# Kernel optimization log

Hardware: AMD Instinct MI355X
Metric: run time of the kernel (lower is better)

## Reference

```python
import jax, jax.numpy as jnp
import numpy as np

K_WAVE = 15.0  # wavenumber k from source
EPS_R = 1e-8   # epsilon in dr/dn denominator from source


def bessel_j1(x):
    # Numerical-Recipes rational/asymptotic approximation of J1(x).
    ax = jnp.abs(x)
    y = x * x
    num = x * (72362614232.0 + y * (-7895059235.0 + y * (242396853.1 + y * (-2972611.439 + y * (15704.48260 + y * (-30.16036606))))))
    den = 144725228442.0 + y * (2300535178.0 + y * (18583304.74 + y * (99447.43394 + y * (376.9991397 + y))))
    small = num / den
    axs = jnp.maximum(ax, 1e-20)
    z = 8.0 / axs
    y2 = z * z
    xx = axs - 2.356194491
    p1 = 1.0 + y2 * (0.183105e-2 + y2 * (-0.3516396496e-4 + y2 * (0.2457520174e-5 + y2 * (-0.240337019e-6))))
    p2 = 0.04687499995 + y2 * (-0.2002690873e-3 + y2 * (0.8449199096e-5 + y2 * (-0.88228987e-6 + y2 * 0.105787412e-6)))
    large = jnp.sqrt(0.636619772 / axs) * (jnp.cos(xx) * p1 - z * jnp.sin(xx) * p2) * jnp.sign(x)
    return jnp.where(ax < 8.0, small, large)


def bessel_y1(x):
    # Numerical-Recipes approximation of Y1(x), x > 0.
    xs = jnp.maximum(x, 1e-12)
    y = xs * xs
    num = xs * (-4.900604943e13 + y * (1.275274390e13 + y * (-5.153438139e11 + y * (7.349264551e9 + y * (-4.237922726e7 + y * 8.511937935e4)))))
    den = 2.499580570e14 + y * (4.244419664e12 + y * (3.733650367e10 + y * (2.245904002e8 + y * (1.020426050e6 + y * (3.549632885e3 + y)))))
    small = num / den + 0.636619772 * (bessel_j1(xs) * jnp.log(xs) - 1.0 / xs)
    z = 8.0 / xs
    y2 = z * z
    xx = xs - 2.356194491
    p1 = 1.0 + y2 * (0.183105e-2 + y2 * (-0.3516396496e-4 + y2 * (0.2457520174e-5 + y2 * (-0.240337019e-6))))
    p2 = 0.04687499995 + y2 * (-0.2002690873e-3 + y2 * (0.8449199096e-5 + y2 * (-0.88228987e-6 + y2 * 0.105787412e-6)))
    large = jnp.sqrt(0.636619772 / xs) * (jnp.sin(xx) * p1 + z * jnp.cos(xx) * p2)
    return jnp.where(xs < 8.0, small, large)


def _mlp(pts, W1, b1, W2, b2, W3, b3, W4, b4, W5, b5):
    h = jnp.tanh(pts @ W1 + b1)
    h = jnp.tanh(h @ W2 + b2)
    h = jnp.tanh(h @ W3 + b3)
    h = jnp.tanh(h @ W4 + b4)
    return (h @ W5 + b5)[:, 0]  # [M]


def setup_inputs() -> dict:
    key = jax.random.key(0)
    ks = jax.random.split(key, 12)
    N = 1024            # points per side (source uses 50)
    P = 16384           # query points
    H = 50              # hidden width (source default)
    cords = np.linspace(0.0001, 0.9999, N, dtype=np.float32)
    z = np.zeros(N, dtype=np.float32)
    o = np.ones(N, dtype=np.float32)
    top = np.stack([cords, o], 1)
    bottom = np.stack([cords, z], 1)
    left = np.stack([z, cords], 1)
    right = np.stack([o, cords], 1)
    boundary_points = jnp.asarray(np.concatenate([top, bottom, left, right], 0))  # [4N,2]
    nrm = np.concatenate([
        np.stack([z, o], 1),    # top normal (0,1)
        np.stack([z, -o], 1),   # bottom (0,-1)
        np.stack([-o, z], 1),   # left (-1,0)
        np.stack([o, z], 1),    # right (1,0)
    ], 0)
    normals = jnp.asarray(nrm)
    dy = jnp.float32(1.0 / (N - 1))
    points = jax.random.uniform(ks[0], (P, 2), dtype=jnp.float32)
    def lin(k, fin, fout):
        lim = np.sqrt(6.0 / (fin + fout)).astype(np.float32)
        return jax.random.uniform(k, (fin, fout), minval=-lim, maxval=lim, dtype=jnp.float32)
    return {
        'points': points,
        'boundary_points': boundary_points,
        'normals': normals,
        'dy': dy,
        'W1': lin(ks[1], 2, H), 'b1': jnp.zeros((H,), jnp.float32),
        'W2': lin(ks[2], H, H), 'b2': jnp.zeros((H,), jnp.float32),
        'W3': lin(ks[3], H, H), 'b3': jnp.zeros((H,), jnp.float32),
        'W4': lin(ks[4], H, H), 'b4': jnp.zeros((H,), jnp.float32),
        'W5': lin(ks[5], H, 1), 'b5': jnp.zeros((1,), jnp.float32),
    }


def reference(points, boundary_points, normals, dy, W1, b1, W2, b2, W3, b3, W4, b4, W5, b5):
    # density values on the boundary from the MLP
    h_vals = _mlp(boundary_points, W1, b1, W2, b2, W3, b3, W4, b4, W5, b5)  # [M]
    # pairwise geometry: [P, M, 2]
    diff = points[:, None, :] - boundary_points[None, :, :]
    r = jnp.sqrt(jnp.sum(diff * diff, axis=-1))               # [P, M]
    dr_dn = jnp.sum(diff * normals[None, :, :], axis=-1) / (r + EPS_R)
    # Re[-(i/4)*k*H1^{(1)}(k r)] = (k/4)*Y1(k r); output is the real part only,
    # so the J1 (imaginary) component never contributes to the returned value.
    y1 = jax.lax.stop_gradient(bessel_y1(K_WAVE * r))  # hankel term is detached in torch (numpy round-trip)
    green_real = 0.25 * K_WAVE * y1 * dr_dn                   # [P, M]
    u_real = jnp.sum(green_real * h_vals[None, :], axis=-1) * dy  # [P]
    return u_real
```

## Files before the change

### kernel.cpp

```cpp
#include <hip/hip_runtime.h>
#include <math.h>

#define H 50
#define TPB 256
#define N_TAB 1368
#define K_WAVE 15.0f
#define NSIDE 1024
#define STEP (0.9998f / 1023.0f)
#define NB_MLP 1024
#define NB_TAB 6

__device__ float y1_f(float x) {
    float inv_x = __fdividef(1.0f, x);
    float y = x * x;
    float nj = fmaf(y, -30.16036606f, 15704.48260f);
    nj = fmaf(y, nj, -2972611.439f);
    nj = fmaf(y, nj, 242396853.1f);
    nj = fmaf(y, nj, -7895059235.0f);
    nj = fmaf(y, nj, 72362614232.0f);
    nj *= x;
    float dj = y + 376.9991397f;
    dj = fmaf(y, dj, 99447.43394f);
    dj = fmaf(y, dj, 18583304.74f);
    dj = fmaf(y, dj, 2300535178.0f);
    dj = fmaf(y, dj, 144725228442.0f);
    float j1 = __fdividef(nj, dj);
    float ny1 = fmaf(y, 8.511937935e4f, -4.237922726e7f);
    ny1 = fmaf(y, ny1, 7.349264551e9f);
    ny1 = fmaf(y, ny1, -5.153438139e11f);
    ny1 = fmaf(y, ny1, 1.275274390e13f);
    ny1 = fmaf(y, ny1, -4.900604943e13f);
    ny1 *= x;
    float dy1 = y + 3.549632885e3f;
    dy1 = fmaf(y, dy1, 1.020426050e6f);
    dy1 = fmaf(y, dy1, 2.245904002e8f);
    dy1 = fmaf(y, dy1, 3.733650367e10f);
    dy1 = fmaf(y, dy1, 4.244419664e12f);
    dy1 = fmaf(y, dy1, 2.499580570e14f);
    float y1_small = __fdividef(ny1, dy1) + 0.636619772f * (j1 * __logf(x) - inv_x);
    float z = 8.0f * inv_x;
    float y2 = z * z;
    float xx = x - 2.356194491f;
    float p1 = fmaf(y2, -0.240337019e-6f, 0.2457520174e-5f);
    p1 = fmaf(y2, p1, -0.3516396496e-4f);
    p1 = fmaf(y2, p1, 0.183105e-2f);
    p1 = fmaf(y2, p1, 1.0f);
    float p2 = fmaf(y2, 0.105787412e-6f, -0.88228987e-6f);
    p2 = fmaf(y2, p2, 0.8449199096e-5f);
    p2 = fmaf(y2, p2, -0.2002690873e-3f);
    p2 = fmaf(y2, p2, 0.04687499995f);
    float s, c;
    __sincosf(xx, &s, &c);
    float y1_large = sqrtf(0.636619772f * inv_x) * fmaf(s, p1, z * c * p2);
    return (x < 8.0f) ? y1_small : y1_large;
}

__global__ __launch_bounds__(256) void prep_kernel(
    const float* __restrict__ bp,
    const float* __restrict__ W1, const float* __restrict__ b1,
    const float* __restrict__ W2, const float* __restrict__ b2,
    const float* __restrict__ W3, const float* __restrict__ b3,
    const float* __restrict__ W4, const float* __restrict__ b4,
    const float* __restrict__ W5, const float* __restrict__ b5,
    const float* __restrict__ dyp,
    float* __restrict__ h_out, float2* __restrict__ tab, int M)
{
    if (blockIdx.x >= NB_MLP) {
        int i = (blockIdx.x - NB_MLP) * 256 + threadIdx.x;
        if (i < N_TAB) {
            const float dxt = 1.0f / 64.0f;
            float x0 = (float)i * dxt, x1 = (float)(i + 1) * dxt;
            float g0 = (i == 0) ? -0.63661977f : x0 * y1_f(x0);
            float g1 = x1 * y1_f(x1);
            tab[i] = make_float2(g0, g1 - g0);
        }
        return;
    }
    __shared__ float ha[4][56];
    __shared__ float hb[4][56];
    int wave = threadIdx.x >> 6;
    int j = threadIdx.x & 63;
    int m = blockIdx.x * 4 + wave;
    if (m >= M) return;
    float px = bp[2 * m], py = bp[2 * m + 1];

    if (j < H) {
        ha[wave][j] = tanhf(fmaf(px, W1[j], fmaf(py, W1[H + j], b1[j])));
    }
    __syncthreads();
    if (j < H) {
        float s = b2[j];
        #pragma unroll
        for (int i = 0; i < H; ++i) s = fmaf(ha[wave][i], W2[i * H + j], s);
        hb[wave][j] = tanhf(s);
    }
    __syncthreads();
    if (j < H) {
        float s = b3[j];
        #pragma unroll
        for (int i = 0; i < H; ++i) s = fmaf(hb[wave][i], W3[i * H + j], s);
        ha[wave][j] = tanhf(s);
    }
    __syncthreads();
    if (j < H) {
        float s = b4[j];
        #pragma unroll
        for (int i = 0; i < H; ++i) s = fmaf(ha[wave][i], W4[i * H + j], s);
        hb[wave][j] = tanhf(s);
    }
    __syncthreads();
    if (j == 0) {
        float s = b5[0];
        #pragma unroll
        for (int i = 0; i < H; ++i) s = fmaf(hb[wave][i], W5[i], s);
        h_out[m] = s * (0.25f * dyp[0]);
    }
}

__global__ __launch_bounds__(TPB, 8) void pair_kernel(
    const float* __restrict__ pts,
    const float* __restrict__ hs,
    const float2* __restrict__ tab,
    float* __restrict__ out, int P)
{
    __shared__ float2 lt[N_TAB];
    for (int i = threadIdx.x; i < N_TAB; i += TPB) lt[i] = tab[i];
    __syncthreads();

    int wave = threadIdx.x >> 6;
    int lane = threadIdx.x & 63;
    int p0 = blockIdx.x * 8 + wave * 2;

    float pxa = pts[2 * p0],     pya = pts[2 * p0 + 1];
    float pxb = pts[2 * p0 + 2], pyb = pts[2 * p0 + 3];

    const float SCL = 64.0f * K_WAVE;
    float tota = 0.0f, totb = 0.0f;

    #pragma unroll
    for (int side = 0; side < 4; ++side) {
        float va, vb, wa, wb, sgn;
        if (side == 0)      { va = pxa; wa = pya - 1.0f; vb = pxb; wb = pyb - 1.0f; sgn =  1.0f; }
        else if (side == 1) { va = pxa; wa = pya;        vb = pxb; wb = pyb;        sgn = -1.0f; }
        else if (side == 2) { va = pya; wa = pxa;        vb = pyb; wb = pxb;        sgn = -1.0f; }
        else                { va = pya; wa = pxa - 1.0f; vb = pyb; wb = pxb - 1.0f; sgn =  1.0f; }
        float w2a = fmaxf(wa * wa, 1e-12f);
        float w2b = fmaxf(wb * wb, 1e-12f);
        float base = 0.0001f + (float)lane * STEP;
        float dxa = va - base;
        float dxb = vb - base;
        const float* hp = hs + side * NSIDE + lane;
        float acca = 0.0f, accb = 0.0f;
        #pragma unroll 4
        for (int t = 0; t < NSIDE / 64; ++t) {
            float hm = hp[t * 64];
            {
                float r2 = fmaf(dxa, dxa, w2a);
                float ir = __builtin_amdgcn_rsqf(r2);
                float tt = (r2 * ir) * SCL;
                int   i  = (int)tt;
                float f  = tt - (float)i;
                float2 gs = lt[i];
                acca = fmaf(fmaf(f, gs.y, gs.x) * hm, ir * ir, acca);
                dxa -= 64.0f * STEP;
            }
            {
                float r2 = fmaf(dxb, dxb, w2b);
                float ir = __builtin_amdgcn_rsqf(r2);
                float tt = (r2 * ir) * SCL;
                int   i  = (int)tt;
                float f  = tt - (float)i;
                float2 gs = lt[i];
                accb = fmaf(fmaf(f, gs.y, gs.x) * hm, ir * ir, accb);
                dxb -= 64.0f * STEP;
            }
        }
        tota = fmaf(acca, wa * sgn, tota);
        totb = fmaf(accb, wb * sgn, totb);
    }

    #pragma unroll
    for (int off = 32; off >= 1; off >>= 1) {
        tota += __shfl_xor(tota, off, 64);
        totb += __shfl_xor(totb, off, 64);
    }
    if (lane == 0) {
        out[p0]     = tota;
        out[p0 + 1] = totb;
    }
}

extern "C" void kernel_launch(void* const* d_in, const int* in_sizes, int n_in,
                              void* d_out, int out_size, void* d_ws, size_t ws_size,
                              hipStream_t stream) {
    const float* pts = (const float*)d_in[0];
    const float* bp  = (const float*)d_in[1];
    const float* dyp = (const float*)d_in[3];
    const float* W1 = (const float*)d_in[4];  const float* b1 = (const float*)d_in[5];
    const float* W2 = (const float*)d_in[6];  const float* b2 = (const float*)d_in[7];
    const float* W3 = (const float*)d_in[8];  const float* b3 = (const float*)d_in[9];
    const float* W4 = (const float*)d_in[10]; const float* b4 = (const float*)d_in[11];
    const float* W5 = (const float*)d_in[12]; const float* b5 = (const float*)d_in[13];

    int P = in_sizes[0] / 2;
    int M = in_sizes[1] / 2;

    float*  hs  = (float*)d_ws;
    float2* tab = (float2*)((char*)d_ws + (size_t)M * 4);

    prep_kernel<<<dim3(NB_MLP + NB_TAB), dim3(256), 0, stream>>>(
        bp, W1, b1, W2, b2, W3, b3, W4, b4, W5, b5, dyp, hs, tab, M);

    pair_kernel<<<dim3(P / 8), dim3(TPB), 0, stream>>>(
        pts, hs, tab, (float*)d_out, P);
}
```

Baseline: 113.8 us.

## Index Green's table by float bits of r^2, dropping rsqrt per pair

The interpolation table is rebuilt over u = r^2, with nodes spaced by the top bits of the float representation (exponent plus 6 mantissa bits). Each table entry stores G(u) = x*Y1(x)/u, so the 1/r^2 factor is folded into the table. The inner loop no longer needs rsqrt, a float-to-int conversion or the ir*ir multiply. It extracts the index by shifting the bit pattern and uses the low mantissa bits as the fractional weight. The trade-off is a larger LDS table (2304 vs 1368 float2 entries), piecewise-linear interpolation on a log-like grid that changes accuracy, and recomputing dx from t instead of decrementing it.

```diff
diff --git a/kernel.cpp b/kernel.cpp
--- a/kernel.cpp
+++ b/kernel.cpp
@@ -3,12 +3,13 @@
 
 #define H 50
 #define TPB 256
-#define N_TAB 1368
 #define K_WAVE 15.0f
 #define NSIDE 1024
 #define STEP (0.9998f / 1023.0f)
 #define NB_MLP 1024
-#define NB_TAB 6
+#define N_TAB 2304
+#define NB_TAB 9
+#define IDX_BASE 5952
 
 __device__ float y1_f(float x) {
     float inv_x = __fdividef(1.0f, x);
@@ -55,6 +56,12 @@
     return (x < 8.0f) ? y1_small : y1_large;
 }
 
+__device__ float G_of_u_node(int i) {
+    float u = __uint_as_float((unsigned)(IDX_BASE + i) << 17);
+    float x = K_WAVE * sqrtf(u);
+    return __fdividef(x * y1_f(x), u);
+}
+
 __global__ __launch_bounds__(256) void prep_kernel(
     const float* __restrict__ bp,
     const float* __restrict__ W1, const float* __restrict__ b1,
@@ -68,11 +75,9 @@
     if (blockIdx.x >= NB_MLP) {
         int i = (blockIdx.x - NB_MLP) * 256 + threadIdx.x;
         if (i < N_TAB) {
-            const float dxt = 1.0f / 64.0f;
-            float x0 = (float)i * dxt, x1 = (float)(i + 1) * dxt;
-            float g0 = (i == 0) ? -0.63661977f : x0 * y1_f(x0);
-            float g1 = x1 * y1_f(x1);
-            tab[i] = make_float2(g0, g1 - g0);
+            float g0 = G_of_u_node(i);
+            float g1 = G_of_u_node(i + 1);
+            tab[i] = make_float2(g0, (g1 - g0) * (1.0f / 131072.0f));
         }
         return;
     }
@@ -134,8 +139,8 @@
     float pxa = pts[2 * p0],     pya = pts[2 * p0 + 1];
     float pxb = pts[2 * p0 + 2], pyb = pts[2 * p0 + 3];
 
-    const float SCL = 64.0f * K_WAVE;
     float tota = 0.0f, totb = 0.0f;
+    float base = fmaf((float)lane, STEP, 0.0001f);
 
     #pragma unroll
     for (int side = 0; side < 4; ++side) {
@@ -144,35 +149,33 @@
         else if (side == 1) { va = pxa; wa = pya;        vb = pxb; wb = pyb;        sgn = -1.0f; }
         else if (side == 2) { va = pya; wa = pxa;        vb = pyb; wb = pxb;        sgn = -1.0f; }
         else                { va = pya; wa = pxa - 1.0f; vb = pyb; wb = pxb - 1.0f; sgn =  1.0f; }
-        float w2a = fmaxf(wa * wa, 1e-12f);
-        float w2b = fmaxf(wb * wb, 1e-12f);
-        float base = 0.0001f + (float)lane * STEP;
-        float dxa = va - base;
-        float dxb = vb - base;
+        float w2a = wa * wa;
+        float w2b = wb * wb;
+        float d0a = va - base;
+        float d0b = vb - base;
         const float* hp = hs + side * NSIDE + lane;
         float acca = 0.0f, accb = 0.0f;
         #pragma unroll 4
         for (int t = 0; t < NSIDE / 64; ++t) {
             float hm = hp[t * 64];
+            float ct = (float)(t * 64) * STEP;
             {
-                float r2 = fmaf(dxa, dxa, w2a);
-                float ir = __builtin_amdgcn_rsqf(r2);
-                float tt = (r2 * ir) * SCL;
-                int   i  = (int)tt;
-                float f  = tt - (float)i;
+                float dx = d0a - ct;
+                float u = fmaxf(fmaf(dx, dx, w2a), 6.0e-11f);
+                unsigned b = __float_as_uint(u);
+                int   i  = (int)(b >> 17) - IDX_BASE;
+                float f  = (float)(b & 0x1FFFFu);
                 float2 gs = lt[i];
-                acca = fmaf(fmaf(f, gs.y, gs.x) * hm, ir * ir, acca);
-                dxa -= 64.0f * STEP;
+                acca = fmaf(fmaf(f, gs.y, gs.x), hm, acca);
             }
             {
-                float r2 = fmaf(dxb, dxb, w2b);
-                float ir = __builtin_amdgcn_rsqf(r2);
-                float tt = (r2 * ir) * SCL;
-                int   i  = (int)tt;
-                float f  = tt - (float)i;
+                float dx = d0b - ct;
+                float u = fmaxf(fmaf(dx, dx, w2b), 6.0e-11f);
+                unsigned b = __float_as_uint(u);
+                int   i  = (int)(b >> 17) - IDX_BASE;
+                float f  = (float)(b & 0x1FFFFu);
                 float2 gs = lt[i];
-                accb = fmaf(fmaf(f, gs.y, gs.x) * hm, ir * ir, accb);
-                dxb -= 64.0f * STEP;
+                accb = fmaf(fmaf(f, gs.y, gs.x), hm, accb);
             }
         }
         tota = fmaf(acca, wa * sgn, tota);
```

Result: faster. 108.3 us (-4.9%).
